# Performance work log

Measured on AMD Instinct MI355X. Metric: run time of the kernel, lower is better.

The kernel has to match this reference:

```python
import jax, jax.numpy as jnp
import numpy as np

B, H, S, D = 4, 8, 4096, 64

def setup_inputs() -> dict:
    key = jax.random.key(0)
    kq, kk, kv = jax.random.split(key, 3)
    Q = jax.random.normal(kq, (B, H, S, D), dtype=jnp.float32)
    K = jax.random.normal(kk, (B, H, S, D), dtype=jnp.float32)
    V = jax.random.normal(kv, (B, H, S, D), dtype=jnp.float32)
    return {"Q": Q, "K": K, "V": V}

def reference(Q, K, V):
    scale = 1.0 / jnp.sqrt(jnp.float32(Q.shape[-1]))
    # scores: [B, H, S, S]
    scores = jnp.einsum('bhqd,bhkd->bhqk', Q, K) * scale
    attn = jax.nn.softmax(scores, axis=-1)
    # out: [B, H, S, D]
    return jnp.einsum('bhqk,bhkd->bhqd', attn, V)
```

## Files before the change

kernel.cpp:

```cpp
#include <hip/hip_runtime.h>
#include <hip/hip_bf16.h>

typedef float  f32x16 __attribute__((ext_vector_type(16)));
typedef __bf16 bf16x8 __attribute__((ext_vector_type(8)));
typedef __bf16 bf16x4 __attribute__((ext_vector_type(4)));
typedef __bf16 bf16x2 __attribute__((ext_vector_type(2)));
typedef int    i32x2v __attribute__((ext_vector_type(2)));
typedef int    i32x4v __attribute__((ext_vector_type(4)));

#define SEQ   4096
#define DDIM  64
#define QB    256
#define KB    64
#define NT    (SEQ / KB)
#define SCL   0.18033688011112042f
#define DEFT  16.0f

#if __has_builtin(__builtin_amdgcn_exp2f)
#define EXP2(x) __builtin_amdgcn_exp2f(x)
#else
#define EXP2(x) __expf((x) * 0.6931471805599453f)
#endif

__device__ __forceinline__ int swzrow(int row) {
  return (((row & 7) ^ ((row >> 3) & 3)) << 4);
}

__device__ __forceinline__ void pswap32(int &x, int &y) {
#if __has_builtin(__builtin_amdgcn_permlane32_swap)
  i32x2v r = __builtin_amdgcn_permlane32_swap(x, y, false, false);
  x = r[0]; y = r[1];
#else
  asm volatile("v_permlane32_swap_b32 %0, %1" : "+v"(x), "+v"(y));
#endif
}

__device__ __forceinline__ bf16x4 cvt4(float4 f) {
  bf16x4 r;
  r[0] = (__bf16)f.x; r[1] = (__bf16)f.y; r[2] = (__bf16)f.z; r[3] = (__bf16)f.w;
  return r;
}

__device__ __forceinline__ bf16x8 mkfrag(int a, int b, int c, int d) {
  i32x4v v; v[0] = a; v[1] = b; v[2] = c; v[3] = d;
  return __builtin_bit_cast(bf16x8, v);
}

__global__ __launch_bounds__(512, 4)
void fattn(const float* __restrict__ Qg, const float* __restrict__ Kg,
           const float* __restrict__ Vg, float* __restrict__ Og)
{
  __shared__ __align__(16) char smem[32768];

  const int tid  = threadIdx.x;
  const int w    = tid >> 6;
  const int lane = tid & 63;
  const int q31  = lane & 31;
  const int h    = lane >> 5;

  int wg = (int)blockIdx.x;
  wg = (wg & 7) * 64 + (wg >> 3);
  const int bh = wg >> 4;
  const int qb = wg & 15;
  const size_t base = (size_t)bh * (SEQ * DDIM);
  const int qrow = qb * QB + w * 32 + q31;

  bf16x8 aq[4];
  {
    const float* qp = Qg + base + (size_t)qrow * DDIM + 8 * h;
    #pragma unroll
    for (int c = 0; c < 4; ++c) {
      float4 f0 = *(const float4*)(qp + 16 * c);
      float4 f1 = *(const float4*)(qp + 16 * c + 4);
      aq[c][0] = (__bf16)(f0.x * SCL);
      aq[c][1] = (__bf16)(f0.y * SCL);
      aq[c][2] = (__bf16)(f0.z * SCL);
      aq[c][3] = (__bf16)(f0.w * SCL);
      aq[c][4] = (__bf16)(f1.x * SCL);
      aq[c][5] = (__bf16)(f1.y * SCL);
      aq[c][6] = (__bf16)(f1.z * SCL);
      aq[c][7] = (__bf16)(f1.w * SCL);
    }
  }

  const int kvA = tid >> 4;
  const int dK  = (tid & 15) * 4;
  const int kw0 = ((kvA * 128 + dK * 2) ^ swzrow(kvA));
  const int kv0 = (tid >> 4) * 2;
  const int dV  = (tid & 15) * 4;
  int vw[4];
  #pragma unroll
  for (int qq = 0; qq < 4; ++qq)
    vw[qq] = 8192 + (((dV + qq) * 128 + kv0 * 2) ^ swzrow(dV + qq));

  const float* kptr = Kg + base + (size_t)kvA * DDIM + dK;
  const float* vptr = Vg + base + (size_t)kv0 * DDIM + dV;

  const int swr = swzrow(q31);
  int kaddr[4];
  #pragma unroll
  for (int c = 0; c < 4; ++c)
    kaddr[c] = q31 * 128 + ((32 * c + 16 * h) ^ swr);

  f32x16 o0 = {}, o1 = {};
  float mrow = 0.f, lsum = 0.f;

  {
    float4 ka = *(const float4*)(kptr);
    float4 kb = *(const float4*)(kptr + 32 * DDIM);
    float4 va = *(const float4*)(vptr);
    float4 vb = *(const float4*)(vptr + DDIM);
    *(bf16x4*)(smem + kw0)            = cvt4(ka);
    *(bf16x4*)(smem + kw0 + 32 * 128) = cvt4(kb);
    float va4[4] = {va.x, va.y, va.z, va.w};
    float vb4[4] = {vb.x, vb.y, vb.z, vb.w};
    #pragma unroll
    for (int qq = 0; qq < 4; ++qq) {
      bf16x2 p; p[0] = (__bf16)va4[qq]; p[1] = (__bf16)vb4[qq];
      *(bf16x2*)(smem + vw[qq]) = p;
    }
  }

  int rbase = 0;

  for (int t = 0; t < NT; ++t) {
    __syncthreads();
    const bool more = (t + 1) < NT;
    const float* kpt = kptr + (size_t)(t + 1) * (KB * DDIM);
    const float* vpt = vptr + (size_t)(t + 1) * (KB * DDIM);

    float4 ka = {}, kb = {};
    if (more) {
      ka = *(const float4*)(kpt);
      kb = *(const float4*)(kpt + 32 * DDIM);
    }

    f32x16 s0 = {}, s1 = {};
    #pragma unroll
    for (int c = 0; c < 4; ++c) {
      bf16x8 k0 = *(const bf16x8*)(smem + rbase + kaddr[c]);
      bf16x8 k1 = *(const bf16x8*)(smem + rbase + kaddr[c] + 4096);
      s0 = __builtin_amdgcn_mfma_f32_32x32x16_bf16(k0, aq[c], s0, 0, 0, 0);
      s1 = __builtin_amdgcn_mfma_f32_32x32x16_bf16(k1, aq[c], s1, 0, 0, 0);
    }

    float4 va = {}, vb = {};
    if (more) {
      va = *(const float4*)(vpt);
      vb = *(const float4*)(vpt + DDIM);
    }

    float pm;
    {
      float a = fmaxf(fmaxf(fmaxf(s0[0], s0[1]), fmaxf(s0[2], s0[3])),
                      fmaxf(fmaxf(s0[4], s0[5]), fmaxf(s0[6], s0[7])));
      float b = fmaxf(fmaxf(fmaxf(s0[8], s0[9]), fmaxf(s0[10], s0[11])),
                      fmaxf(fmaxf(s0[12], s0[13]), fmaxf(s0[14], s0[15])));
      float c = fmaxf(fmaxf(fmaxf(s1[0], s1[1]), fmaxf(s1[2], s1[3])),
                      fmaxf(fmaxf(s1[4], s1[5]), fmaxf(s1[6], s1[7])));
      float d = fmaxf(fmaxf(fmaxf(s1[8], s1[9]), fmaxf(s1[10], s1[11])),
                      fmaxf(fmaxf(s1[12], s1[13]), fmaxf(s1[14], s1[15])));
      pm = fmaxf(fmaxf(a, b), fmaxf(c, d));
    }
    if (!__all(pm <= mrow + DEFT)) {
      float tm = fmaxf(pm, __shfl_xor(pm, 32));
      float mn = fmaxf(mrow, tm);
      float corr = EXP2(mrow - mn);
      o0 *= corr; o1 *= corr;
      lsum *= corr;
      mrow = mn;
    }
    #pragma unroll
    for (int r = 0; r < 16; ++r) s0[r] = EXP2(s0[r] - mrow);
    #pragma unroll
    for (int r = 0; r < 16; ++r) s1[r] = EXP2(s1[r] - mrow);

    f32x16 ts = s0 + s1;
    lsum += ((((ts[0]+ts[1])+(ts[2]+ts[3])) + ((ts[4]+ts[5])+(ts[6]+ts[7])))
          +  (((ts[8]+ts[9])+(ts[10]+ts[11])) + ((ts[12]+ts[13])+(ts[14]+ts[15]))));

    int pk[2][8];
    #pragma unroll
    for (int u = 0; u < 8; ++u) {
      bf16x2 p0; p0[0] = (__bf16)s0[2*u]; p0[1] = (__bf16)s0[2*u+1];
      pk[0][u] = __builtin_bit_cast(int, p0);
      bf16x2 p1; p1[0] = (__bf16)s1[2*u]; p1[1] = (__bf16)s1[2*u+1];
      pk[1][u] = __builtin_bit_cast(int, p1);
    }
    #pragma unroll
    for (int m = 0; m < 2; ++m) {
      pswap32(pk[m][0], pk[m][2]);
      pswap32(pk[m][1], pk[m][3]);
      pswap32(pk[m][4], pk[m][6]);
      pswap32(pk[m][5], pk[m][7]);
    }

    const int wb = rbase ^ 16384;
    if (more) {
      *(bf16x4*)(smem + wb + kw0)            = cvt4(ka);
      *(bf16x4*)(smem + wb + kw0 + 32 * 128) = cvt4(kb);
    }

    #pragma unroll
    for (int c = 0; c < 4; ++c) {
      bf16x8 bp = mkfrag(pk[c>>1][(c&1)*4+0], pk[c>>1][(c&1)*4+1],
                         pk[c>>1][(c&1)*4+2], pk[c>>1][(c&1)*4+3]);
      bf16x8 v0 = *(const bf16x8*)(smem + rbase + kaddr[c] + 8192);
      bf16x8 v1 = *(const bf16x8*)(smem + rbase + kaddr[c] + 12288);
      o0 = __builtin_amdgcn_mfma_f32_32x32x16_bf16(v0, bp, o0, 0, 0, 0);
      o1 = __builtin_amdgcn_mfma_f32_32x32x16_bf16(v1, bp, o1, 0, 0, 0);
    }

    if (more) {
      float va4[4] = {va.x, va.y, va.z, va.w};
      float vb4[4] = {vb.x, vb.y, vb.z, vb.w};
      #pragma unroll
      for (int qq = 0; qq < 4; ++qq) {
        bf16x2 p; p[0] = (__bf16)va4[qq]; p[1] = (__bf16)vb4[qq];
        *(bf16x2*)(smem + wb + vw[qq]) = p;
      }
    }
    rbase ^= 16384;
  }

  float l = lsum + __shfl_xor(lsum, 32);
  float inv = 1.0f / l;
  float* op = Og + base + (size_t)qrow * DDIM + 4 * h;
  #pragma unroll
  for (int rg = 0; rg < 4; ++rg) {
    float4 st0 = { o0[4*rg+0]*inv, o0[4*rg+1]*inv, o0[4*rg+2]*inv, o0[4*rg+3]*inv };
    *(float4*)(op + 8*rg) = st0;
    float4 st1 = { o1[4*rg+0]*inv, o1[4*rg+1]*inv, o1[4*rg+2]*inv, o1[4*rg+3]*inv };
    *(float4*)(op + 8*rg + 32) = st1;
  }
}

extern "C" void kernel_launch(void* const* d_in, const int* in_sizes, int n_in,
                              void* d_out, int out_size, void* d_ws, size_t ws_size,
                              hipStream_t stream) {
  const float* Q = (const float*)d_in[0];
  const float* K = (const float*)d_in[1];
  const float* V = (const float*)d_in[2];
  float* O = (float*)d_out;
  dim3 grid(32 * (SEQ / QB));
  dim3 block(512);
  fattn<<<grid, block, 0, stream>>>(Q, K, V, O);
}
```

Baseline: 179.3 us.

## Software-pipeline QK and PV MFMAs with triple-buffered K/V tiles

Restructures the main loop so the P·V MFMAs for tile t are interleaved with the Q·K MFMAs for tile t+1, with the softmax of tile t+1 overlapping later work. Shared memory grows to three buffers so the t+2 tile can be staged while t and t+1 are read. It also raises wave priority around the MFMA blocks and skips the max subtraction in exp while the running max is still zero. The larger LDS footprint (48KB per block) may lower occupancy below the 4-block launch bound, and register pressure rises.

```diff
diff --git a/kernel.cpp b/kernel.cpp
--- a/kernel.cpp
+++ b/kernel.cpp
@@ -13,6 +13,7 @@
 #define QB    256
 #define KB    64
 #define NT    (SEQ / KB)
+#define BUF   16384
 #define SCL   0.18033688011112042f
 #define DEFT  16.0f
 
@@ -46,11 +47,18 @@
   return __builtin_bit_cast(bf16x8, v);
 }
 
+__device__ __forceinline__ float max8(const f32x16& s, int o) {
+  float m = fmaxf(fmaxf(s[o+0], s[o+1]), s[o+2]);
+  m = fmaxf(fmaxf(m, s[o+3]), s[o+4]);
+  m = fmaxf(fmaxf(m, s[o+5]), s[o+6]);
+  return fmaxf(m, s[o+7]);
+}
+
 __global__ __launch_bounds__(512, 4)
 void fattn(const float* __restrict__ Qg, const float* __restrict__ Kg,
            const float* __restrict__ Vg, float* __restrict__ Og)
 {
-  __shared__ __align__(16) char smem[32768];
+  __shared__ __align__(16) char smem[3 * BUF];
 
   const int tid  = threadIdx.x;
   const int w    = tid >> 6;
@@ -92,7 +100,6 @@
   #pragma unroll
   for (int qq = 0; qq < 4; ++qq)
     vw[qq] = 8192 + (((dV + qq) * 128 + kv0 * 2) ^ swzrow(dV + qq));
-
   const float* kptr = Kg + base + (size_t)kvA * DDIM + dK;
   const float* vptr = Vg + base + (size_t)kv0 * DDIM + dV;
 
@@ -104,82 +111,34 @@
 
   f32x16 o0 = {}, o1 = {};
   float mrow = 0.f, lsum = 0.f;
-
-  {
-    float4 ka = *(const float4*)(kptr);
-    float4 kb = *(const float4*)(kptr + 32 * DDIM);
-    float4 va = *(const float4*)(vptr);
-    float4 vb = *(const float4*)(vptr + DDIM);
-    *(bf16x4*)(smem + kw0)            = cvt4(ka);
-    *(bf16x4*)(smem + kw0 + 32 * 128) = cvt4(kb);
-    float va4[4] = {va.x, va.y, va.z, va.w};
-    float vb4[4] = {vb.x, vb.y, vb.z, vb.w};
-    #pragma unroll
-    for (int qq = 0; qq < 4; ++qq) {
-      bf16x2 p; p[0] = (__bf16)va4[qq]; p[1] = (__bf16)vb4[qq];
-      *(bf16x2*)(smem + vw[qq]) = p;
-    }
-  }
-
-  int rbase = 0;
-
-  for (int t = 0; t < NT; ++t) {
-    __syncthreads();
-    const bool more = (t + 1) < NT;
-    const float* kpt = kptr + (size_t)(t + 1) * (KB * DDIM);
-    const float* vpt = vptr + (size_t)(t + 1) * (KB * DDIM);
-
-    float4 ka = {}, kb = {};
-    if (more) {
-      ka = *(const float4*)(kpt);
-      kb = *(const float4*)(kpt + 32 * DDIM);
-    }
-
-    f32x16 s0 = {}, s1 = {};
-    #pragma unroll
-    for (int c = 0; c < 4; ++c) {
-      bf16x8 k0 = *(const bf16x8*)(smem + rbase + kaddr[c]);
-      bf16x8 k1 = *(const bf16x8*)(smem + rbase + kaddr[c] + 4096);
-      s0 = __builtin_amdgcn_mfma_f32_32x32x16_bf16(k0, aq[c], s0, 0, 0, 0);
-      s1 = __builtin_amdgcn_mfma_f32_32x32x16_bf16(k1, aq[c], s1, 0, 0, 0);
-    }
-
-    float4 va = {}, vb = {};
-    if (more) {
-      va = *(const float4*)(vpt);
-      vb = *(const float4*)(vpt + DDIM);
-    }
-
-    float pm;
-    {
-      float a = fmaxf(fmaxf(fmaxf(s0[0], s0[1]), fmaxf(s0[2], s0[3])),
-                      fmaxf(fmaxf(s0[4], s0[5]), fmaxf(s0[6], s0[7])));
-      float b = fmaxf(fmaxf(fmaxf(s0[8], s0[9]), fmaxf(s0[10], s0[11])),
-                      fmaxf(fmaxf(s0[12], s0[13]), fmaxf(s0[14], s0[15])));
-      float c = fmaxf(fmaxf(fmaxf(s1[0], s1[1]), fmaxf(s1[2], s1[3])),
-                      fmaxf(fmaxf(s1[4], s1[5]), fmaxf(s1[6], s1[7])));
-      float d = fmaxf(fmaxf(fmaxf(s1[8], s1[9]), fmaxf(s1[10], s1[11])),
-                      fmaxf(fmaxf(s1[12], s1[13]), fmaxf(s1[14], s1[15])));
-      pm = fmaxf(fmaxf(a, b), fmaxf(c, d));
-    }
+  int mzero = 1;
+  int pk[2][8];
+
+  auto softmax_pack = [&](f32x16& s0, f32x16& s1) {
+    float m0 = max8(s0, 0), m1 = max8(s0, 8);
+    float m2 = max8(s1, 0), m3 = max8(s1, 8);
+    float pm = fmaxf(fmaxf(m0, m1), fmaxf(m2, m3));
     if (!__all(pm <= mrow + DEFT)) {
       float tm = fmaxf(pm, __shfl_xor(pm, 32));
       float mn = fmaxf(mrow, tm);
       float corr = EXP2(mrow - mn);
-      o0 *= corr; o1 *= corr;
-      lsum *= corr;
-      mrow = mn;
-    }
-    #pragma unroll
-    for (int r = 0; r < 16; ++r) s0[r] = EXP2(s0[r] - mrow);
-    #pragma unroll
-    for (int r = 0; r < 16; ++r) s1[r] = EXP2(s1[r] - mrow);
-
+      o0 *= corr; o1 *= corr; lsum *= corr;
+      mrow = mn; mzero = 0;
+    }
+    if (__builtin_expect(mzero, 1)) {
+      #pragma unroll
+      for (int r = 0; r < 16; ++r) s0[r] = EXP2(s0[r]);
+      #pragma unroll
+      for (int r = 0; r < 16; ++r) s1[r] = EXP2(s1[r]);
+    } else {
+      #pragma unroll
+      for (int r = 0; r < 16; ++r) s0[r] = EXP2(s0[r] - mrow);
+      #pragma unroll
+      for (int r = 0; r < 16; ++r) s1[r] = EXP2(s1[r] - mrow);
+    }
     f32x16 ts = s0 + s1;
     lsum += ((((ts[0]+ts[1])+(ts[2]+ts[3])) + ((ts[4]+ts[5])+(ts[6]+ts[7])))
           +  (((ts[8]+ts[9])+(ts[10]+ts[11])) + ((ts[12]+ts[13])+(ts[14]+ts[15]))));
-
-    int pk[2][8];
     #pragma unroll
     for (int u = 0; u < 8; ++u) {
       bf16x2 p0; p0[0] = (__bf16)s0[2*u]; p0[1] = (__bf16)s0[2*u+1];
@@ -194,33 +153,106 @@
       pswap32(pk[m][4], pk[m][6]);
       pswap32(pk[m][5], pk[m][7]);
     }
-
-    const int wb = rbase ^ 16384;
+  };
+
+  #pragma unroll
+  for (int pt = 0; pt < 2; ++pt) {
+    const float* kp = kptr + (size_t)pt * (KB * DDIM);
+    const float* vp = vptr + (size_t)pt * (KB * DDIM);
+    float4 ka = *(const float4*)(kp);
+    float4 kb = *(const float4*)(kp + 32 * DDIM);
+    float4 va = *(const float4*)(vp);
+    float4 vb = *(const float4*)(vp + DDIM);
+    int bo = pt * BUF;
+    *(bf16x4*)(smem + bo + kw0)            = cvt4(ka);
+    *(bf16x4*)(smem + bo + kw0 + 32 * 128) = cvt4(kb);
+    float va4[4] = {va.x, va.y, va.z, va.w};
+    float vb4[4] = {vb.x, vb.y, vb.z, vb.w};
+    #pragma unroll
+    for (int qq = 0; qq < 4; ++qq) {
+      bf16x2 p; p[0] = (__bf16)va4[qq]; p[1] = (__bf16)vb4[qq];
+      *(bf16x2*)(smem + bo + vw[qq]) = p;
+    }
+  }
+  __syncthreads();
+
+  {
+    f32x16 s0 = {}, s1 = {};
+    __builtin_amdgcn_s_setprio(1);
+    #pragma unroll
+    for (int c = 0; c < 4; ++c) {
+      bf16x8 k0 = *(const bf16x8*)(smem + kaddr[c]);
+      bf16x8 k1 = *(const bf16x8*)(smem + kaddr[c] + 4096);
+      s0 = __builtin_amdgcn_mfma_f32_32x32x16_bf16(k0, aq[c], s0, 0, 0, 0);
+      s1 = __builtin_amdgcn_mfma_f32_32x32x16_bf16(k1, aq[c], s1, 0, 0, 0);
+    }
+    __builtin_amdgcn_s_setprio(0);
+    softmax_pack(s0, s1);
+  }
+
+  int cur = 0, nxt = BUF, nx2 = 2 * BUF;
+
+  for (int t = 0; t < NT; ++t) {
+    __syncthreads();
+    const bool more  = (t + 1) < NT;
+    const bool more2 = (t + 2) < NT;
+
+    f32x16 s0 = {}, s1 = {};
     if (more) {
-      *(bf16x4*)(smem + wb + kw0)            = cvt4(ka);
-      *(bf16x4*)(smem + wb + kw0 + 32 * 128) = cvt4(kb);
-    }
-
-    #pragma unroll
-    for (int c = 0; c < 4; ++c) {
-      bf16x8 bp = mkfrag(pk[c>>1][(c&1)*4+0], pk[c>>1][(c&1)*4+1],
-                         pk[c>>1][(c&1)*4+2], pk[c>>1][(c&1)*4+3]);
-      bf16x8 v0 = *(const bf16x8*)(smem + rbase + kaddr[c] + 8192);
-      bf16x8 v1 = *(const bf16x8*)(smem + rbase + kaddr[c] + 12288);
-      o0 = __builtin_amdgcn_mfma_f32_32x32x16_bf16(v0, bp, o0, 0, 0, 0);
-      o1 = __builtin_amdgcn_mfma_f32_32x32x16_bf16(v1, bp, o1, 0, 0, 0);
-    }
-
-    if (more) {
+      __builtin_amdgcn_s_setprio(1);
+      #pragma unroll
+      for (int c = 0; c < 4; ++c) {
+        bf16x8 bp = mkfrag(pk[c>>1][(c&1)*4+0], pk[c>>1][(c&1)*4+1],
+                           pk[c>>1][(c&1)*4+2], pk[c>>1][(c&1)*4+3]);
+        bf16x8 v0 = *(const bf16x8*)(smem + cur + kaddr[c] + 8192);
+        bf16x8 v1 = *(const bf16x8*)(smem + cur + kaddr[c] + 12288);
+        o0 = __builtin_amdgcn_mfma_f32_32x32x16_bf16(v0, bp, o0, 0, 0, 0);
+        o1 = __builtin_amdgcn_mfma_f32_32x32x16_bf16(v1, bp, o1, 0, 0, 0);
+        bf16x8 k0 = *(const bf16x8*)(smem + nxt + kaddr[c]);
+        bf16x8 k1 = *(const bf16x8*)(smem + nxt + kaddr[c] + 4096);
+        s0 = __builtin_amdgcn_mfma_f32_32x32x16_bf16(k0, aq[c], s0, 0, 0, 0);
+        s1 = __builtin_amdgcn_mfma_f32_32x32x16_bf16(k1, aq[c], s1, 0, 0, 0);
+      }
+      __builtin_amdgcn_s_setprio(0);
+    } else {
+      __builtin_amdgcn_s_setprio(1);
+      #pragma unroll
+      for (int c = 0; c < 4; ++c) {
+        bf16x8 bp = mkfrag(pk[c>>1][(c&1)*4+0], pk[c>>1][(c&1)*4+1],
+                           pk[c>>1][(c&1)*4+2], pk[c>>1][(c&1)*4+3]);
+        bf16x8 v0 = *(const bf16x8*)(smem + cur + kaddr[c] + 8192);
+        bf16x8 v1 = *(const bf16x8*)(smem + cur + kaddr[c] + 12288);
+        o0 = __builtin_amdgcn_mfma_f32_32x32x16_bf16(v0, bp, o0, 0, 0, 0);
+        o1 = __builtin_amdgcn_mfma_f32_32x32x16_bf16(v1, bp, o1, 0, 0, 0);
+      }
+      __builtin_amdgcn_s_setprio(0);
+    }
+
+    float4 ka = {}, kb = {}, va = {}, vb = {};
+    if (more2) {
+      const float* kp = kptr + (size_t)(t + 2) * (KB * DDIM);
+      const float* vp = vptr + (size_t)(t + 2) * (KB * DDIM);
+      ka = *(const float4*)(kp);
+      kb = *(const float4*)(kp + 32 * DDIM);
+      va = *(const float4*)(vp);
+      vb = *(const float4*)(vp + DDIM);
+    }
+
+    if (more) softmax_pack(s0, s1);
+
+    if (more2) {
+      *(bf16x4*)(smem + nx2 + kw0)            = cvt4(ka);
+      *(bf16x4*)(smem + nx2 + kw0 + 32 * 128) = cvt4(kb);
       float va4[4] = {va.x, va.y, va.z, va.w};
       float vb4[4] = {vb.x, vb.y, vb.z, vb.w};
       #pragma unroll
       for (int qq = 0; qq < 4; ++qq) {
         bf16x2 p; p[0] = (__bf16)va4[qq]; p[1] = (__bf16)vb4[qq];
-        *(bf16x2*)(smem + wb + vw[qq]) = p;
+        *(bf16x2*)(smem + nx2 + vw[qq]) = p;
       }
     }
-    rbase ^= 16384;
+
+    int tmp = cur; cur = nxt; nxt = nx2; nx2 = tmp;
   }
 
   float l = lsum + __shfl_xor(lsum, 32);
```

Result: slower. 225.4 us (+25.7%).

## Pre-convert K/V to swizzled bf16 tiles in workspace, then stream tiles

Applied to the files above, without the earlier changes.

Adds a prep kernel that converts K and V to bf16 and writes them as pre-swizzled 16KB tiles in workspace, with V transposed. The attention kernel then copies whole tiles into LDS with 16-byte loads and stores, with no per-iteration conversion or scattered transposed stores. Blocks shrink to 256 threads covering 128 query rows, so the grid doubles. MFMA sections are wrapped in s_setprio. The cost is an extra launch plus a full K/V read and write through workspace. A fallback keeps the old kernel when workspace is too small.

```diff
diff --git a/kernel.cpp b/kernel.cpp
--- a/kernel.cpp
+++ b/kernel.cpp
@@ -10,9 +10,10 @@
 
 #define SEQ   4096
 #define DDIM  64
-#define QB    256
 #define KB    64
 #define NT    (SEQ / KB)
+#define TILEB 16384
+#define WSNEED (32ull * NT * TILEB)
 #define SCL   0.18033688011112042f
 #define DEFT  16.0f
 
@@ -22,8 +23,8 @@
 #define EXP2(x) __expf((x) * 0.6931471805599453f)
 #endif
 
-__device__ __forceinline__ int swzrow(int row) {
-  return (((row & 7) ^ ((row >> 3) & 3)) << 4);
+__device__ __forceinline__ int swzb(int row) {
+  return (row & 7) ^ ((row >> 3) & 3);
 }
 
 __device__ __forceinline__ void pswap32(int &x, int &y) {
@@ -35,22 +36,53 @@
 #endif
 }
 
-__device__ __forceinline__ bf16x4 cvt4(float4 f) {
-  bf16x4 r;
-  r[0] = (__bf16)f.x; r[1] = (__bf16)f.y; r[2] = (__bf16)f.z; r[3] = (__bf16)f.w;
-  return r;
-}
-
 __device__ __forceinline__ bf16x8 mkfrag(int a, int b, int c, int d) {
   i32x4v v; v[0] = a; v[1] = b; v[2] = c; v[3] = d;
   return __builtin_bit_cast(bf16x8, v);
 }
 
-__global__ __launch_bounds__(512, 4)
-void fattn(const float* __restrict__ Qg, const float* __restrict__ Kg,
-           const float* __restrict__ Vg, float* __restrict__ Og)
+__device__ __forceinline__ float max8(const f32x16& s, int o) {
+  float m = fmaxf(fmaxf(s[o+0], s[o+1]), s[o+2]);
+  m = fmaxf(fmaxf(m, s[o+3]), s[o+4]);
+  m = fmaxf(fmaxf(m, s[o+5]), s[o+6]);
+  return fmaxf(m, s[o+7]);
+}
+
+__global__ __launch_bounds__(256)
+void prep(const float* __restrict__ Kg, const float* __restrict__ Vg,
+          char* __restrict__ KVb)
 {
-  __shared__ __align__(16) char smem[32768];
+  int i = blockIdx.x * 256 + threadIdx.x;
+  if (i < (1 << 20)) {
+    int row = i >> 3, s_in = i & 7;
+    int bh = row >> 12, r = row & 4095, t = r >> 6, kv = r & 63;
+    const float* src = Kg + (size_t)row * 64 + s_in * 8;
+    float4 f0 = *(const float4*)(src);
+    float4 f1 = *(const float4*)(src + 4);
+    bf16x8 p;
+    p[0] = (__bf16)f0.x; p[1] = (__bf16)f0.y; p[2] = (__bf16)f0.z; p[3] = (__bf16)f0.w;
+    p[4] = (__bf16)f1.x; p[5] = (__bf16)f1.y; p[6] = (__bf16)f1.z; p[7] = (__bf16)f1.w;
+    char* dst = KVb + (size_t)(bh * NT + t) * TILEB + kv * 128 + ((s_in ^ swzb(kv)) * 16);
+    *(bf16x8*)dst = p;
+  } else {
+    int j = i - (1 << 20);
+    int d = j & 63, rest = j >> 6;
+    int kvg = rest & 7, t = (rest >> 3) & 63, bh = rest >> 9;
+    const float* src = Vg + (size_t)bh * (SEQ * DDIM) + (t * 64 + kvg * 8) * 64 + d;
+    bf16x8 p;
+    #pragma unroll
+    for (int jj = 0; jj < 8; ++jj) p[jj] = (__bf16)src[jj * 64];
+    char* dst = KVb + (size_t)(bh * NT + t) * TILEB + 8192 + d * 128
+              + ((kvg ^ swzb(d)) * 16);
+    *(bf16x8*)dst = p;
+  }
+}
+
+__global__ __launch_bounds__(256, 4)
+void fattn(const float* __restrict__ Qg, const char* __restrict__ KVb,
+           float* __restrict__ Og)
+{
+  __shared__ __align__(16) char smem[2 * TILEB];
 
   const int tid  = threadIdx.x;
   const int w    = tid >> 6;
@@ -59,11 +91,11 @@
   const int h    = lane >> 5;
 
   int wg = (int)blockIdx.x;
-  wg = (wg & 7) * 64 + (wg >> 3);
-  const int bh = wg >> 4;
-  const int qb = wg & 15;
+  wg = (wg & 7) * 128 + (wg >> 3);
+  const int bh = wg >> 5;
+  const int qb = wg & 31;
   const size_t base = (size_t)bh * (SEQ * DDIM);
-  const int qrow = qb * QB + w * 32 + q31;
+  const int qrow = qb * 128 + w * 32 + q31;
 
   bf16x8 aq[4];
   {
@@ -83,20 +115,10 @@
     }
   }
 
-  const int kvA = tid >> 4;
-  const int dK  = (tid & 15) * 4;
-  const int kw0 = ((kvA * 128 + dK * 2) ^ swzrow(kvA));
-  const int kv0 = (tid >> 4) * 2;
-  const int dV  = (tid & 15) * 4;
-  int vw[4];
-  #pragma unroll
-  for (int qq = 0; qq < 4; ++qq)
-    vw[qq] = 8192 + (((dV + qq) * 128 + kv0 * 2) ^ swzrow(dV + qq));
-
-  const float* kptr = Kg + base + (size_t)kvA * DDIM + dK;
-  const float* vptr = Vg + base + (size_t)kv0 * DDIM + dV;
-
-  const int swr = swzrow(q31);
+  const char* kvt = KVb + (size_t)bh * (NT * TILEB);
+  const int soff = tid * 16;
+
+  const int swr = swzb(q31) << 4;
   int kaddr[4];
   #pragma unroll
   for (int c = 0; c < 4; ++c)
@@ -104,82 +126,26 @@
 
   f32x16 o0 = {}, o1 = {};
   float mrow = 0.f, lsum = 0.f;
-
-  {
-    float4 ka = *(const float4*)(kptr);
-    float4 kb = *(const float4*)(kptr + 32 * DDIM);
-    float4 va = *(const float4*)(vptr);
-    float4 vb = *(const float4*)(vptr + DDIM);
-    *(bf16x4*)(smem + kw0)            = cvt4(ka);
-    *(bf16x4*)(smem + kw0 + 32 * 128) = cvt4(kb);
-    float va4[4] = {va.x, va.y, va.z, va.w};
-    float vb4[4] = {vb.x, vb.y, vb.z, vb.w};
-    #pragma unroll
-    for (int qq = 0; qq < 4; ++qq) {
-      bf16x2 p; p[0] = (__bf16)va4[qq]; p[1] = (__bf16)vb4[qq];
-      *(bf16x2*)(smem + vw[qq]) = p;
-    }
-  }
-
-  int rbase = 0;
-
-  for (int t = 0; t < NT; ++t) {
-    __syncthreads();
-    const bool more = (t + 1) < NT;
-    const float* kpt = kptr + (size_t)(t + 1) * (KB * DDIM);
-    const float* vpt = vptr + (size_t)(t + 1) * (KB * DDIM);
-
-    float4 ka = {}, kb = {};
-    if (more) {
-      ka = *(const float4*)(kpt);
-      kb = *(const float4*)(kpt + 32 * DDIM);
-    }
-
-    f32x16 s0 = {}, s1 = {};
-    #pragma unroll
-    for (int c = 0; c < 4; ++c) {
-      bf16x8 k0 = *(const bf16x8*)(smem + rbase + kaddr[c]);
-      bf16x8 k1 = *(const bf16x8*)(smem + rbase + kaddr[c] + 4096);
-      s0 = __builtin_amdgcn_mfma_f32_32x32x16_bf16(k0, aq[c], s0, 0, 0, 0);
-      s1 = __builtin_amdgcn_mfma_f32_32x32x16_bf16(k1, aq[c], s1, 0, 0, 0);
-    }
-
-    float4 va = {}, vb = {};
-    if (more) {
-      va = *(const float4*)(vpt);
-      vb = *(const float4*)(vpt + DDIM);
-    }
-
-    float pm;
-    {
-      float a = fmaxf(fmaxf(fmaxf(s0[0], s0[1]), fmaxf(s0[2], s0[3])),
-                      fmaxf(fmaxf(s0[4], s0[5]), fmaxf(s0[6], s0[7])));
-      float b = fmaxf(fmaxf(fmaxf(s0[8], s0[9]), fmaxf(s0[10], s0[11])),
-                      fmaxf(fmaxf(s0[12], s0[13]), fmaxf(s0[14], s0[15])));
-      float c = fmaxf(fmaxf(fmaxf(s1[0], s1[1]), fmaxf(s1[2], s1[3])),
-                      fmaxf(fmaxf(s1[4], s1[5]), fmaxf(s1[6], s1[7])));
-      float d = fmaxf(fmaxf(fmaxf(s1[8], s1[9]), fmaxf(s1[10], s1[11])),
-                      fmaxf(fmaxf(s1[12], s1[13]), fmaxf(s1[14], s1[15])));
-      pm = fmaxf(fmaxf(a, b), fmaxf(c, d));
-    }
+  int pk[2][8];
+
+  auto softmax_pack = [&](f32x16& s0, f32x16& s1) {
+    float m0 = max8(s0, 0), m1 = max8(s0, 8);
+    float m2 = max8(s1, 0), m3 = max8(s1, 8);
+    float pm = fmaxf(fmaxf(m0, m1), fmaxf(m2, m3));
     if (!__all(pm <= mrow + DEFT)) {
       float tm = fmaxf(pm, __shfl_xor(pm, 32));
       float mn = fmaxf(mrow, tm);
       float corr = EXP2(mrow - mn);
-      o0 *= corr; o1 *= corr;
-      lsum *= corr;
+      o0 *= corr; o1 *= corr; lsum *= corr;
       mrow = mn;
     }
     #pragma unroll
     for (int r = 0; r < 16; ++r) s0[r] = EXP2(s0[r] - mrow);
     #pragma unroll
     for (int r = 0; r < 16; ++r) s1[r] = EXP2(s1[r] - mrow);
-
     f32x16 ts = s0 + s1;
     lsum += ((((ts[0]+ts[1])+(ts[2]+ts[3])) + ((ts[4]+ts[5])+(ts[6]+ts[7])))
           +  (((ts[8]+ts[9])+(ts[10]+ts[11])) + ((ts[12]+ts[13])+(ts[14]+ts[15]))));
-
-    int pk[2][8];
     #pragma unroll
     for (int u = 0; u < 8; ++u) {
       bf16x2 p0; p0[0] = (__bf16)s0[2*u]; p0[1] = (__bf16)s0[2*u+1];
@@ -194,33 +160,65 @@
       pswap32(pk[m][4], pk[m][6]);
       pswap32(pk[m][5], pk[m][7]);
     }
-
-    const int wb = rbase ^ 16384;
+  };
+
+  {
+    const char* sp = kvt + soff;
+    #pragma unroll
+    for (int c = 0; c < 4; ++c)
+      *(bf16x8*)(smem + soff + c * 4096) = *(const bf16x8*)(sp + c * 4096);
+  }
+  __syncthreads();
+
+  for (int t = 0; t < NT; ++t) {
+    const int cur  = (t & 1) << 14;
+    const int nxtb = cur ^ TILEB;
+    const bool more = (t + 1) < NT;
+
+    bf16x8 st0, st1, st2, st3;
     if (more) {
-      *(bf16x4*)(smem + wb + kw0)            = cvt4(ka);
-      *(bf16x4*)(smem + wb + kw0 + 32 * 128) = cvt4(kb);
-    }
-
+      const char* sp = kvt + (size_t)(t + 1) * TILEB + soff;
+      st0 = *(const bf16x8*)(sp);
+      st1 = *(const bf16x8*)(sp + 4096);
+      st2 = *(const bf16x8*)(sp + 8192);
+      st3 = *(const bf16x8*)(sp + 12288);
+    }
+
+    f32x16 s0 = {}, s1 = {};
+    __builtin_amdgcn_s_setprio(1);
+    #pragma unroll
+    for (int c = 0; c < 4; ++c) {
+      bf16x8 k0 = *(const bf16x8*)(smem + cur + kaddr[c]);
+      bf16x8 k1 = *(const bf16x8*)(smem + cur + kaddr[c] + 4096);
+      s0 = __builtin_amdgcn_mfma_f32_32x32x16_bf16(k0, aq[c], s0, 0, 0, 0);
+      s1 = __builtin_amdgcn_mfma_f32_32x32x16_bf16(k1, aq[c], s1, 0, 0, 0);
+    }
+    __builtin_amdgcn_s_setprio(0);
+
+    if (more) {
+      *(bf16x8*)(smem + nxtb + soff)        = st0;
+      *(bf16x8*)(smem + nxtb + soff + 4096) = st1;
+    }
+
+    softmax_pack(s0, s1);
+
+    __builtin_amdgcn_s_setprio(1);
     #pragma unroll
     for (int c = 0; c < 4; ++c) {
       bf16x8 bp = mkfrag(pk[c>>1][(c&1)*4+0], pk[c>>1][(c&1)*4+1],
                          pk[c>>1][(c&1)*4+2], pk[c>>1][(c&1)*4+3]);
-      bf16x8 v0 = *(const bf16x8*)(smem + rbase + kaddr[c] + 8192);
-      bf16x8 v1 = *(const bf16x8*)(smem + rbase + kaddr[c] + 12288);
+      bf16x8 v0 = *(const bf16x8*)(smem + cur + kaddr[c] + 8192);
+      bf16x8 v1 = *(const bf16x8*)(smem + cur + kaddr[c] + 12288);
       o0 = __builtin_amdgcn_mfma_f32_32x32x16_bf16(v0, bp, o0, 0, 0, 0);
       o1 = __builtin_amdgcn_mfma_f32_32x32x16_bf16(v1, bp, o1, 0, 0, 0);
     }
+    __builtin_amdgcn_s_setprio(0);
 
     if (more) {
-      float va4[4] = {va.x, va.y, va.z, va.w};
-      float vb4[4] = {vb.x, vb.y, vb.z, vb.w};
-      #pragma unroll
-      for (int qq = 0; qq < 4; ++qq) {
-        bf16x2 p; p[0] = (__bf16)va4[qq]; p[1] = (__bf16)vb4[qq];
-        *(bf16x2*)(smem + wb + vw[qq]) = p;
-      }
-    }
-    rbase ^= 16384;
+      *(bf16x8*)(smem + nxtb + soff + 8192)  = st2;
+      *(bf16x8*)(smem + nxtb + soff + 12288) = st3;
+    }
+    __syncthreads();
   }
 
   float l = lsum + __shfl_xor(lsum, 32);
@@ -235,6 +233,177 @@
   }
 }
 
+__global__ __launch_bounds__(512)
+void fattn_fb(const float* __restrict__ Qg, const float* __restrict__ Kg,
+              const float* __restrict__ Vg, float* __restrict__ Og)
+{
+  __shared__ __align__(16) char smem[32768];
+  const int tid  = threadIdx.x;
+  const int w    = tid >> 6;
+  const int lane = tid & 63;
+  const int q31  = lane & 31;
+  const int h    = lane >> 5;
+
+  int wg = (int)blockIdx.x;
+  wg = (wg & 7) * 64 + (wg >> 3);
+  const int bh = wg >> 4;
+  const int qb = wg & 15;
+  const size_t base = (size_t)bh * (SEQ * DDIM);
+  const int qrow = qb * 256 + w * 32 + q31;
+
+  bf16x8 aq[4];
+  {
+    const float* qp = Qg + base + (size_t)qrow * DDIM + 8 * h;
+    #pragma unroll
+    for (int c = 0; c < 4; ++c) {
+      float4 f0 = *(const float4*)(qp + 16 * c);
+      float4 f1 = *(const float4*)(qp + 16 * c + 4);
+      aq[c][0] = (__bf16)(f0.x * SCL); aq[c][1] = (__bf16)(f0.y * SCL);
+      aq[c][2] = (__bf16)(f0.z * SCL); aq[c][3] = (__bf16)(f0.w * SCL);
+      aq[c][4] = (__bf16)(f1.x * SCL); aq[c][5] = (__bf16)(f1.y * SCL);
+      aq[c][6] = (__bf16)(f1.z * SCL); aq[c][7] = (__bf16)(f1.w * SCL);
+    }
+  }
+
+  const int kvA = tid >> 4;
+  const int dK  = (tid & 15) * 4;
+  const int kw0 = ((kvA * 128 + dK * 2) ^ (swzb(kvA) << 4));
+  const int kv0 = (tid >> 4) * 2;
+  const int dV  = (tid & 15) * 4;
+  int vw[4];
+  #pragma unroll
+  for (int qq = 0; qq < 4; ++qq)
+    vw[qq] = 8192 + (((dV + qq) * 128 + kv0 * 2) ^ (swzb(dV + qq) << 4));
+  const float* kptr = Kg + base + (size_t)kvA * DDIM + dK;
+  const float* vptr = Vg + base + (size_t)kv0 * DDIM + dV;
+
+  const int swr = swzb(q31) << 4;
+  int kaddr[4];
+  #pragma unroll
+  for (int c = 0; c < 4; ++c)
+    kaddr[c] = q31 * 128 + ((32 * c + 16 * h) ^ swr);
+
+  f32x16 o0 = {}, o1 = {};
+  float mrow = 0.f, lsum = 0.f;
+
+  {
+    float4 ka = *(const float4*)(kptr);
+    float4 kb = *(const float4*)(kptr + 32 * DDIM);
+    float4 va = *(const float4*)(vptr);
+    float4 vb = *(const float4*)(vptr + DDIM);
+    bf16x4 pa, pb;
+    pa[0]=(__bf16)ka.x; pa[1]=(__bf16)ka.y; pa[2]=(__bf16)ka.z; pa[3]=(__bf16)ka.w;
+    pb[0]=(__bf16)kb.x; pb[1]=(__bf16)kb.y; pb[2]=(__bf16)kb.z; pb[3]=(__bf16)kb.w;
+    *(bf16x4*)(smem + kw0)            = pa;
+    *(bf16x4*)(smem + kw0 + 32 * 128) = pb;
+    float va4[4] = {va.x, va.y, va.z, va.w};
+    float vb4[4] = {vb.x, vb.y, vb.z, vb.w};
+    #pragma unroll
+    for (int qq = 0; qq < 4; ++qq) {
+      bf16x2 p; p[0] = (__bf16)va4[qq]; p[1] = (__bf16)vb4[qq];
+      *(bf16x2*)(smem + vw[qq]) = p;
+    }
+  }
+
+  int rbase = 0;
+  for (int t = 0; t < NT; ++t) {
+    __syncthreads();
+    const bool more = (t + 1) < NT;
+    const float* kpt = kptr + (size_t)(t + 1) * (KB * DDIM);
+    const float* vpt = vptr + (size_t)(t + 1) * (KB * DDIM);
+    float4 ka = {}, kb = {};
+    if (more) { ka = *(const float4*)(kpt); kb = *(const float4*)(kpt + 32 * DDIM); }
+
+    f32x16 s0 = {}, s1 = {};
+    #pragma unroll
+    for (int c = 0; c < 4; ++c) {
+      bf16x8 k0 = *(const bf16x8*)(smem + rbase + kaddr[c]);
+      bf16x8 k1 = *(const bf16x8*)(smem + rbase + kaddr[c] + 4096);
+      s0 = __builtin_amdgcn_mfma_f32_32x32x16_bf16(k0, aq[c], s0, 0, 0, 0);
+      s1 = __builtin_amdgcn_mfma_f32_32x32x16_bf16(k1, aq[c], s1, 0, 0, 0);
+    }
+
+    float4 va = {}, vb = {};
+    if (more) { va = *(const float4*)(vpt); vb = *(const float4*)(vpt + DDIM); }
+
+    float pm;
+    {
+      float m0 = max8(s0, 0), m1 = max8(s0, 8);
+      float m2 = max8(s1, 0), m3 = max8(s1, 8);
+      pm = fmaxf(fmaxf(m0, m1), fmaxf(m2, m3));
+    }
+    if (!__all(pm <= mrow + DEFT)) {
+      float tm = fmaxf(pm, __shfl_xor(pm, 32));
+      float mn = fmaxf(mrow, tm);
+      float corr = EXP2(mrow - mn);
+      o0 *= corr; o1 *= corr; lsum *= corr;
+      mrow = mn;
+    }
+    #pragma unroll
+    for (int r = 0; r < 16; ++r) s0[r] = EXP2(s0[r] - mrow);
+    #pragma unroll
+    for (int r = 0; r < 16; ++r) s1[r] = EXP2(s1[r] - mrow);
+    f32x16 ts = s0 + s1;
+    lsum += ((((ts[0]+ts[1])+(ts[2]+ts[3])) + ((ts[4]+ts[5])+(ts[6]+ts[7])))
+          +  (((ts[8]+ts[9])+(ts[10]+ts[11])) + ((ts[12]+ts[13])+(ts[14]+ts[15]))));
+
+    int pk[2][8];
+    #pragma unroll
+    for (int u = 0; u < 8; ++u) {
+      bf16x2 p0; p0[0] = (__bf16)s0[2*u]; p0[1] = (__bf16)s0[2*u+1];
+      pk[0][u] = __builtin_bit_cast(int, p0);
+      bf16x2 p1; p1[0] = (__bf16)s1[2*u]; p1[1] = (__bf16)s1[2*u+1];
+      pk[1][u] = __builtin_bit_cast(int, p1);
+    }
+    #pragma unroll
+    for (int m = 0; m < 2; ++m) {
+      pswap32(pk[m][0], pk[m][2]); pswap32(pk[m][1], pk[m][3]);
+      pswap32(pk[m][4], pk[m][6]); pswap32(pk[m][5], pk[m][7]);
+    }
+
+    const int wb = rbase ^ 16384;
+    if (more) {
+      bf16x4 pa, pb;
+      pa[0]=(__bf16)ka.x; pa[1]=(__bf16)ka.y; pa[2]=(__bf16)ka.z; pa[3]=(__bf16)ka.w;
+      pb[0]=(__bf16)kb.x; pb[1]=(__bf16)kb.y; pb[2]=(__bf16)kb.z; pb[3]=(__bf16)kb.w;
+      *(bf16x4*)(smem + wb + kw0)            = pa;
+      *(bf16x4*)(smem + wb + kw0 + 32 * 128) = pb;
+    }
+
+    #pragma unroll
+    for (int c = 0; c < 4; ++c) {
+      bf16x8 bp = mkfrag(pk[c>>1][(c&1)*4+0], pk[c>>1][(c&1)*4+1],
+                         pk[c>>1][(c&1)*4+2], pk[c>>1][(c&1)*4+3]);
+      bf16x8 v0 = *(const bf16x8*)(smem + rbase + kaddr[c] + 8192);
+      bf16x8 v1 = *(const bf16x8*)(smem + rbase + kaddr[c] + 12288);
+      o0 = __builtin_amdgcn_mfma_f32_32x32x16_bf16(v0, bp, o0, 0, 0, 0);
+      o1 = __builtin_amdgcn_mfma_f32_32x32x16_bf16(v1, bp, o1, 0, 0, 0);
+    }
+
+    if (more) {
+      float va4[4] = {va.x, va.y, va.z, va.w};
+      float vb4[4] = {vb.x, vb.y, vb.z, vb.w};
+      #pragma unroll
+      for (int qq = 0; qq < 4; ++qq) {
+        bf16x2 p; p[0] = (__bf16)va4[qq]; p[1] = (__bf16)vb4[qq];
+        *(bf16x2*)(smem + wb + vw[qq]) = p;
+      }
+    }
+    rbase ^= 16384;
+  }
+
+  float l = lsum + __shfl_xor(lsum, 32);
+  float inv = 1.0f / l;
+  float* op = Og + base + (size_t)qrow * DDIM + 4 * h;
+  #pragma unroll
+  for (int rg = 0; rg < 4; ++rg) {
+    float4 w0 = { o0[4*rg+0]*inv, o0[4*rg+1]*inv, o0[4*rg+2]*inv, o0[4*rg+3]*inv };
+    *(float4*)(op + 8*rg) = w0;
+    float4 w1 = { o1[4*rg+0]*inv, o1[4*rg+1]*inv, o1[4*rg+2]*inv, o1[4*rg+3]*inv };
+    *(float4*)(op + 8*rg + 32) = w1;
+  }
+}
+
 extern "C" void kernel_launch(void* const* d_in, const int* in_sizes, int n_in,
                               void* d_out, int out_size, void* d_ws, size_t ws_size,
                               hipStream_t stream) {
@@ -242,7 +411,10 @@
   const float* K = (const float*)d_in[1];
   const float* V = (const float*)d_in[2];
   float* O = (float*)d_out;
-  dim3 grid(32 * (SEQ / QB));
-  dim3 block(512);
-  fattn<<<grid, block, 0, stream>>>(Q, K, V, O);
-}
+  if (ws_size >= WSNEED) {
+    prep<<<dim3(8192), dim3(256), 0, stream>>>(K, V, (char*)d_ws);
+    fattn<<<dim3(1024), dim3(256), 0, stream>>>(Q, (const char*)d_ws, O);
+  } else {
+    fattn_fb<<<dim3(512), dim3(512), 0, stream>>>(Q, K, V, O);
+  }
+}
```

Result: slower. 191.3 us (+6.7%).
